# Kernel tuning notes

Measured on AMD Instinct MI355X. Metric: run time of the kernel, lower is better.

## Reference

```python
import jax, jax.numpy as jnp
import numpy as np

D_MODEL = 1040
N_HEADS = 16
FEAT = 32            # feature_dim
HEAD_DIM = 65        # d_model // num_heads; must equal 2*FEAT+1 for the z-division to broadcast
EPS = 1e-9


def setup_inputs() -> dict:
    key = jax.random.key(0)
    k1, k2, k3, k4, k5, k6 = jax.random.split(key, 6)
    B, S = 4, 4096
    scale = 1.0 / np.sqrt(D_MODEL)
    return {
        "hidden_states": jax.random.normal(k1, (B, S, D_MODEL), dtype=jnp.float32),
        "attention_mask": jax.random.randint(k2, (B, S), 0, 2, dtype=jnp.int32),
        "Wq": jax.random.normal(k3, (D_MODEL, N_HEADS * FEAT), dtype=jnp.float32) * scale,
        "Wk": jax.random.normal(k4, (D_MODEL, N_HEADS * FEAT), dtype=jnp.float32) * scale,
        "Wv": jax.random.normal(k5, (D_MODEL, N_HEADS * HEAD_DIM), dtype=jnp.float32) * scale,
        "Wo": jax.random.normal(k6, (N_HEADS * HEAD_DIM, D_MODEL), dtype=jnp.float32) * scale,
    }


def _phi(x):
    # polynomial feature map: [1, x, 0.5*x^2] -> last dim 2*FEAT+1
    return jnp.concatenate([jnp.ones_like(x[..., :1]), x, 0.5 * x * x], axis=-1)


def reference(hidden_states, attention_mask, Wq, Wk, Wv, Wo):
    B, S, _ = hidden_states.shape
    # projections -> [B, H, S, d]
    q = (hidden_states @ Wq).reshape(B, S, N_HEADS, FEAT).transpose(0, 2, 1, 3)
    k = (hidden_states @ Wk).reshape(B, S, N_HEADS, FEAT).transpose(0, 2, 1, 3)
    v = (hidden_states @ Wv).reshape(B, S, N_HEADS, HEAD_DIM).transpose(0, 2, 1, 3)
    q = _phi(q)  # [B, H, S, D] with D = 2*FEAT+1
    k = _phi(k)
    # linear attention: KV state then query it
    kv = jnp.einsum('bhnd,bhne->bhde', k, v)        # [B, H, D, HEAD_DIM]
    qkv = jnp.einsum('bhnd,bhde->bhne', q, kv)      # [B, H, S, HEAD_DIM]
    # z = einsum('bhnd,bhne->bhne', q, k.sum(n, keepdim)) with size-1 broadcast on n:
    # contracts d of q against k.sum's d-slot, i.e. (sum_d q) outer (sum_n k)
    z = jnp.sum(q, axis=-1, keepdims=True) * jnp.sum(k, axis=2, keepdims=True)  # [B,H,S,D]
    out = qkv / (z + EPS)                            # requires HEAD_DIM == D
    out = jnp.where(attention_mask[:, None, :, None] == 0, 0.0, out)
    out = out.transpose(0, 2, 1, 3).reshape(B, S, N_HEADS * HEAD_DIM)
    return out @ Wo
```

## Files before the change

kernel.cpp:

```cpp
#include <hip/hip_runtime.h>
#include <hip/hip_bf16.h>

typedef unsigned short ushort_t;
typedef unsigned int uint_t;

#define S_LEN 4096
#define BATCH 4
#define DMODEL 1040
#define KPAD 1056
#define KO 1152
#define NPADW 1152
#define M_TOK 16384
#define KVSPLIT 16

using f32x4 = __attribute__((ext_vector_type(4))) float;
using bf16x8 = __attribute__((ext_vector_type(8))) __bf16;
using f16x8 = __attribute__((ext_vector_type(8))) _Float16;

__device__ __forceinline__ void splitf16(float x, ushort_t& h, ushort_t& l) {
  _Float16 hf = (_Float16)x;
  float r = (x - (float)hf) * 4096.0f;
  _Float16 lf = (_Float16)r;
  h = __builtin_bit_cast(ushort_t, hf);
  l = __builtin_bit_cast(ushort_t, lf);
}

typedef const __attribute__((address_space(1))) unsigned int* gas_u32p;
typedef __attribute__((address_space(3))) unsigned int* las_u32p;
__device__ __forceinline__ void gload_lds16(const ushort_t* g, ushort_t* l) {
  __builtin_amdgcn_global_load_lds((gas_u32p)g, (las_u32p)l, 16, 0, 0);
}

__device__ __forceinline__ void tile_map(int lid, int NT, int PPX, int& m0, int& n0) {
  const int x = lid & 7, pos = lid >> 3;
  const int mi = pos / NT, ni = pos - mi * NT;
  m0 = (x * PPX + mi) * 128;
  n0 = ni * 128;
}

union pack8 { ushort_t u[8]; uint4 v; };

__global__ __launch_bounds__(256) void split_hs_kernel(const float* __restrict__ hs,
                                                       ushort_t* __restrict__ hh,
                                                       ushort_t* __restrict__ hl) {
  const int C8 = KPAD / 8;
  int idx = blockIdx.x * 256 + threadIdx.x;
  if (idx >= M_TOK * C8) return;
  int row = idx / C8, col = (idx % C8) * 8;
  pack8 ph, pl;
  if (col < DMODEL) {
    const float* p = &hs[(size_t)row * DMODEL + col];
#pragma unroll
    for (int j = 0; j < 8; ++j) splitf16(p[j], ph.u[j], pl.u[j]);
  } else {
#pragma unroll
    for (int j = 0; j < 8; ++j) { ph.u[j] = 0; pl.u[j] = 0; }
  }
  size_t o = (size_t)row * KPAD + col;
  *reinterpret_cast<uint4*>(&hh[o]) = ph.v;
  *reinterpret_cast<uint4*>(&hl[o]) = pl.v;
}

__global__ __launch_bounds__(256) void split_wqk_kernel(const float* __restrict__ Wq,
                                                        const float* __restrict__ Wk,
                                                        ushort_t* __restrict__ th,
                                                        ushort_t* __restrict__ tl) {
  const int C8 = KPAD / 8;
  int idx = blockIdx.x * 256 + threadIdx.x;
  if (idx >= 1024 * C8) return;
  int n = idx / C8, k = (idx % C8) * 8;
  pack8 ph, pl;
#pragma unroll
  for (int j = 0; j < 8; ++j) {
    int kk = k + j;
    float val = 0.f;
    if (kk < DMODEL) val = (n < 512) ? Wq[(size_t)kk * 512 + n] : Wk[(size_t)kk * 512 + (n - 512)];
    splitf16(val, ph.u[j], pl.u[j]);
  }
  size_t o = (size_t)n * KPAD + k;
  *reinterpret_cast<uint4*>(&th[o]) = ph.v;
  *reinterpret_cast<uint4*>(&tl[o]) = pl.v;
}

__global__ __launch_bounds__(256) void split_wv_kernel(const float* __restrict__ Wv,
                                                       ushort_t* __restrict__ th) {
  const int C8 = KPAD / 8;
  int idx = blockIdx.x * 256 + threadIdx.x;
  if (idx >= NPADW * C8) return;
  int n = idx / C8, k = (idx % C8) * 8;
  pack8 ph;
#pragma unroll
  for (int j = 0; j < 8; ++j) {
    int kk = k + j;
    float val = (n < DMODEL && kk < DMODEL) ? Wv[(size_t)kk * DMODEL + n] : 0.f;
    ph.u[j] = __builtin_bit_cast(ushort_t, (_Float16)val);
  }
  *reinterpret_cast<uint4*>(&th[(size_t)n * KPAD + k]) = ph.v;
}

__global__ __launch_bounds__(256) void split_wo_kernel(const float* __restrict__ Wo,
                                                       ushort_t* __restrict__ th) {
  const int C8O = KO / 8;
  int idx = blockIdx.x * 256 + threadIdx.x;
  if (idx >= NPADW * C8O) return;
  int n = idx / C8O, k = (idx % C8O) * 8;
  pack8 ph;
#pragma unroll
  for (int j = 0; j < 8; ++j) {
    int kk = k + j;
    int h = kk / 72, e = kk % 72;
    float val = (n < DMODEL && e < 65) ? Wo[(size_t)(h * 65 + e) * DMODEL + n] : 0.f;
    ph.u[j] = __builtin_bit_cast(ushort_t, __float2bfloat16(val));
  }
  *reinterpret_cast<uint4*>(&th[(size_t)n * KO + k]) = ph.v;
}

__global__ __launch_bounds__(512, 4) void gemm_qk(const ushort_t* __restrict__ Ahg,
                                                  const ushort_t* __restrict__ Alg,
                                                  const ushort_t* __restrict__ Bhg,
                                                  const ushort_t* __restrict__ Blg,
                                                  float* __restrict__ C, int kdim) {
  __shared__ ushort_t Ah[2][4096], Al[2][4096], Bh[2][4096], Bl[2][4096];
  const int t = threadIdx.x;
  const int w = t >> 6, l = t & 63;
  int m0, n0;
  tile_map(blockIdx.x, 8, 16, m0, n0);
  const int wm = w >> 2, wn = w & 3;
  const int row16 = l & 15, g = l >> 4;

  f32x4 acc[4][2], acc2[4][2];
#pragma unroll
  for (int m = 0; m < 4; ++m)
#pragma unroll
    for (int n = 0; n < 2; ++n) { acc[m][n] = (f32x4){0,0,0,0}; acc2[m][n] = (f32x4){0,0,0,0}; }

  const int chunk = t;
  const int r0 = chunk >> 2;
  const int ch0 = (chunk & 3) ^ ((r0 ^ (r0 >> 2)) & 3);

#define STAGE_QK(K0, BUF)                                                       \
  {                                                                             \
    const size_t ga = (size_t)(m0 + r0) * kdim + (K0) + ch0 * 8;                \
    const size_t gb = (size_t)(n0 + r0) * kdim + (K0) + ch0 * 8;                \
    gload_lds16(Ahg + ga, &Ah[BUF][chunk * 8]);                                 \
    gload_lds16(Alg + ga, &Al[BUF][chunk * 8]);                                 \
    gload_lds16(Bhg + gb, &Bh[BUF][chunk * 8]);                                 \
    gload_lds16(Blg + gb, &Bl[BUF][chunk * 8]);                                 \
  }

  STAGE_QK(0, 0);
  __syncthreads();
  for (int k0 = 0, it = 0; k0 < kdim; k0 += 32, ++it) {
    const int cur = it & 1;
    if (k0 + 32 < kdim) STAGE_QK(k0 + 32, cur ^ 1);
    f16x8 fah[4], fal[4], fbh[2], fbl[2];
#pragma unroll
    for (int f = 0; f < 4; ++f) {
      const int ra = wm * 64 + f * 16 + row16;
      const int ca = (g ^ ((ra ^ (ra >> 2)) & 3)) << 3;
      fah[f] = *(const f16x8*)&Ah[cur][ra * 32 + ca];
      fal[f] = *(const f16x8*)&Al[cur][ra * 32 + ca];
    }
#pragma unroll
    for (int f = 0; f < 2; ++f) {
      const int rb = wn * 32 + f * 16 + row16;
      const int cb = (g ^ ((rb ^ (rb >> 2)) & 3)) << 3;
      fbh[f] = *(const f16x8*)&Bh[cur][rb * 32 + cb];
      fbl[f] = *(const f16x8*)&Bl[cur][rb * 32 + cb];
    }
#pragma unroll
    for (int m = 0; m < 4; ++m)
#pragma unroll
      for (int n = 0; n < 2; ++n) {
        acc[m][n]  = __builtin_amdgcn_mfma_f32_16x16x32_f16(fah[m], fbh[n], acc[m][n], 0, 0, 0);
        acc2[m][n] = __builtin_amdgcn_mfma_f32_16x16x32_f16(fah[m], fbl[n], acc2[m][n], 0, 0, 0);
        acc2[m][n] = __builtin_amdgcn_mfma_f32_16x16x32_f16(fal[m], fbh[n], acc2[m][n], 0, 0, 0);
      }
    __syncthreads();
  }
#undef STAGE_QK

  const float S2 = 1.0f / 4096.0f;
#pragma unroll
  for (int m = 0; m < 4; ++m)
#pragma unroll
    for (int n = 0; n < 2; ++n) {
      const int col = n0 + wn * 32 + n * 16 + row16;
      const int rowb = m0 + wm * 64 + m * 16 + g * 4;
#pragma unroll
      for (int i = 0; i < 4; ++i)
        C[(size_t)(rowb + i) * 1024 + col] = acc[m][n][i] + acc2[m][n][i] * S2;
    }
}

__global__ __launch_bounds__(512, 4) void gemm_v(const ushort_t* __restrict__ Ahg,
                                                 const ushort_t* __restrict__ Bhg,
                                                 ushort_t* __restrict__ Cv, int kdim) {
  __shared__ ushort_t Ah[2][4096], Bh[2][4096];
  const int t = threadIdx.x;
  const int w = t >> 6, l = t & 63;
  int m0, n0;
  tile_map(blockIdx.x, 9, 16, m0, n0);
  const int wm = w >> 2, wn = w & 3;
  const int row16 = l & 15, g = l >> 4;

  f32x4 acc[4][2];
#pragma unroll
  for (int m = 0; m < 4; ++m)
#pragma unroll
    for (int n = 0; n < 2; ++n) acc[m][n] = (f32x4){0,0,0,0};

  const int chunk = t;
  const int r0 = chunk >> 2;
  const int ch0 = (chunk & 3) ^ ((r0 ^ (r0 >> 2)) & 3);

#define STAGE_V(K0, BUF)                                                        \
  {                                                                             \
    const size_t ga = (size_t)(m0 + r0) * kdim + (K0) + ch0 * 8;                \
    const size_t gb = (size_t)(n0 + r0) * kdim + (K0) + ch0 * 8;                \
    gload_lds16(Ahg + ga, &Ah[BUF][chunk * 8]);                                 \
    gload_lds16(Bhg + gb, &Bh[BUF][chunk * 8]);                                 \
  }

  STAGE_V(0, 0);
  __syncthreads();
  for (int k0 = 0, it = 0; k0 < kdim; k0 += 32, ++it) {
    const int cur = it & 1;
    if (k0 + 32 < kdim) STAGE_V(k0 + 32, cur ^ 1);
    f16x8 fah[4], fbh[2];
#pragma unroll
    for (int f = 0; f < 4; ++f) {
      const int ra = wm * 64 + f * 16 + row16;
      const int ca = (g ^ ((ra ^ (ra >> 2)) & 3)) << 3;
      fah[f] = *(const f16x8*)&Ah[cur][ra * 32 + ca];
    }
#pragma unroll
    for (int f = 0; f < 2; ++f) {
      const int rb = wn * 32 + f * 16 + row16;
      const int cb = (g ^ ((rb ^ (rb >> 2)) & 3)) << 3;
      fbh[f] = *(const f16x8*)&Bh[cur][rb * 32 + cb];
    }
#pragma unroll
    for (int m = 0; m < 4; ++m)
#pragma unroll
      for (int n = 0; n < 2; ++n)
        acc[m][n] = __builtin_amdgcn_mfma_f32_16x16x32_f16(fah[m], fbh[n], acc[m][n], 0, 0, 0);
    __syncthreads();
  }
#undef STAGE_V

#pragma unroll
  for (int m = 0; m < 4; ++m)
#pragma unroll
    for (int n = 0; n < 2; ++n) {
      const int col = n0 + wn * 32 + n * 16 + row16;
      const int rowb = m0 + wm * 64 + m * 16 + g * 4;
#pragma unroll
      for (int i = 0; i < 4; ++i)
        Cv[(size_t)(rowb + i) * 1152 + col] =
            __builtin_bit_cast(ushort_t, (_Float16)acc[m][n][i]);
    }
}

__global__ __launch_bounds__(512, 4) void gemm_o(const ushort_t* __restrict__ Ahg,
                                                 const ushort_t* __restrict__ Bhg,
                                                 float* __restrict__ C, int kdim) {
  __shared__ ushort_t Ah[2][4096], Bh[2][4096];
  const int t = threadIdx.x;
  const int w = t >> 6, l = t & 63;
  int m0, n0;
  tile_map(blockIdx.x, 9, 16, m0, n0);
  const int wm = w >> 2, wn = w & 3;
  const int row16 = l & 15, g = l >> 4;

  f32x4 acc[4][2];
#pragma unroll
  for (int m = 0; m < 4; ++m)
#pragma unroll
    for (int n = 0; n < 2; ++n) acc[m][n] = (f32x4){0,0,0,0};

  const int chunk = t;
  const int r0 = chunk >> 2;
  const int ch0 = (chunk & 3) ^ ((r0 ^ (r0 >> 2)) & 3);

#define STAGE_O(K0, BUF)                                                        \
  {                                                                             \
    const size_t ga = (size_t)(m0 + r0) * kdim + (K0) + ch0 * 8;                \
    const size_t gb = (size_t)(n0 + r0) * kdim + (K0) + ch0 * 8;                \
    gload_lds16(Ahg + ga, &Ah[BUF][chunk * 8]);                                 \
    gload_lds16(Bhg + gb, &Bh[BUF][chunk * 8]);                                 \
  }

  STAGE_O(0, 0);
  __syncthreads();
  for (int k0 = 0, it = 0; k0 < kdim; k0 += 32, ++it) {
    const int cur = it & 1;
    if (k0 + 32 < kdim) STAGE_O(k0 + 32, cur ^ 1);
    bf16x8 fah[4], fbh[2];
#pragma unroll
    for (int f = 0; f < 4; ++f) {
      const int ra = wm * 64 + f * 16 + row16;
      const int ca = (g ^ ((ra ^ (ra >> 2)) & 3)) << 3;
      fah[f] = *(const bf16x8*)&Ah[cur][ra * 32 + ca];
    }
#pragma unroll
    for (int f = 0; f < 2; ++f) {
      const int rb = wn * 32 + f * 16 + row16;
      const int cb = (g ^ ((rb ^ (rb >> 2)) & 3)) << 3;
      fbh[f] = *(const bf16x8*)&Bh[cur][rb * 32 + cb];
    }
#pragma unroll
    for (int m = 0; m < 4; ++m)
#pragma unroll
      for (int n = 0; n < 2; ++n)
        acc[m][n] = __builtin_amdgcn_mfma_f32_16x16x32_bf16(fah[m], fbh[n], acc[m][n], 0, 0, 0);
    __syncthreads();
  }
#undef STAGE_O

#pragma unroll
  for (int m = 0; m < 4; ++m)
#pragma unroll
    for (int n = 0; n < 2; ++n) {
      const int col = n0 + wn * 32 + n * 16 + row16;
      if (col < DMODEL) {
        const int rowb = m0 + wm * 64 + m * 16 + g * 4;
#pragma unroll
        for (int i = 0; i < 4; ++i) C[(size_t)(rowb + i) * DMODEL + col] = acc[m][n][i];
      }
    }
}

__global__ __launch_bounds__(256) void kv_kernel(const float* __restrict__ qk,
                                                 const ushort_t* __restrict__ vbuf,
                                                 float* __restrict__ kvpart,
                                                 float* __restrict__ kspart) {
  const int bh = blockIdx.x;
  const int split = blockIdx.y;
  const int b = bh >> 4, h = bh & 15;
  __shared__ float ks[64][68];
  __shared__ float vs[64][68];
  const int tid = threadIdx.x;
  const int d0 = (tid / 17) * 5;
  const int e0 = (tid % 17) * 4;
  const bool active = (tid < 221);
  float acc[5][4] = {};
  float kcol = 0.f;

  for (int chunk = 0; chunk < 4; ++chunk) {
    const int nb = split * 256 + chunk * 64;
    for (int idx = tid; idx < 64 * 65; idx += 256) {
      const int r = idx / 65, d = idx % 65;
      const size_t row = (size_t)(b * S_LEN + nb + r);
      float val;
      if (d == 0) val = 1.f;
      else if (d <= 32) val = qk[row * 1024 + 512 + h * 32 + (d - 1)];
      else {
        float x = qk[row * 1024 + 512 + h * 32 + (d - 33)];
        val = 0.5f * x * x;
      }
      ks[r][d] = val;
      vs[r][d] = (float)__builtin_bit_cast(_Float16, vbuf[row * 1152 + h * 65 + d]);
    }
    __syncthreads();
    if (active) {
      for (int r = 0; r < 64; ++r) {
        float a[5], v[4];
#pragma unroll
        for (int i = 0; i < 5; ++i) a[i] = ks[r][d0 + i];
#pragma unroll
        for (int j = 0; j < 4; ++j) v[j] = vs[r][e0 + j];
#pragma unroll
        for (int i = 0; i < 5; ++i)
#pragma unroll
          for (int j = 0; j < 4; ++j) acc[i][j] += a[i] * v[j];
      }
    }
    if (tid < 65) {
      float s = 0.f;
      for (int r = 0; r < 64; ++r) s += ks[r][tid];
      kcol += s;
    }
    __syncthreads();
  }

  if (active) {
    float* kvp = kvpart + ((size_t)split * 64 + bh) * 4225;
#pragma unroll
    for (int i = 0; i < 5; ++i)
#pragma unroll
      for (int j = 0; j < 4; ++j) {
        int e = e0 + j;
        if (e < 65) kvp[(d0 + i) * 65 + e] = acc[i][j];
      }
  }
  if (tid < 65) kspart[((size_t)split * 64 + bh) * 65 + tid] = kcol;
}

__global__ __launch_bounds__(256) void kv_reduce(const float* __restrict__ kvpart,
                                                 const float* __restrict__ kspart,
                                                 float* __restrict__ kv,
                                                 float* __restrict__ ksum) {
  const int NKV = 64 * 4225;
  const int NKS = 64 * 65;
  int i = blockIdx.x * 256 + threadIdx.x;
  if (i < NKV) {
    float s = 0.f;
#pragma unroll 8
    for (int p = 0; p < KVSPLIT; ++p) s += kvpart[(size_t)p * NKV + i];
    kv[i] = s;
  } else if (i < NKV + NKS) {
    int j = i - NKV;
    float s = 0.f;
#pragma unroll 8
    for (int p = 0; p < KVSPLIT; ++p) s += kspart[p * NKS + j];
    ksum[j] = s;
  }
}

__global__ __launch_bounds__(256) void qkv_kernel(const float* __restrict__ qk,
                                                  const float* __restrict__ kv,
                                                  const float* __restrict__ ksum,
                                                  const int* __restrict__ mask,
                                                  uint_t* __restrict__ ath32) {
  const int gx = blockIdx.x;
  const int bh = blockIdx.y;
  const int b = bh >> 4, h = bh & 15;
  __shared__ float kvs[65 * 68];
  __shared__ float phis[128][68];
  __shared__ float kss[65];
  __shared__ float qsums[128];
  const int tid = threadIdx.x;

  const float* kvp = kv + (size_t)bh * 4225;
  for (int i = tid; i < 4225; i += 256) kvs[(i / 65) * 68 + (i % 65)] = kvp[i];
  for (int idx = tid; idx < 128 * 32; idx += 256) {
    int tt = idx >> 5, f = idx & 31;
    size_t row = (size_t)(b * S_LEN + gx * 128 + tt);
    float val = qk[row * 1024 + h * 32 + f];
    phis[tt][1 + f] = val;
    phis[tt][33 + f] = 0.5f * val * val;
  }
  if (tid < 128) phis[tid][0] = 1.f;
  if (tid < 65) kss[tid] = ksum[bh * 65 + tid];
  __syncthreads();
  if (tid < 128) {
    float s = 0.f;
    for (int d = 0; d < 65; ++d) s += phis[tid][d];
    qsums[tid] = s;
  }
  __syncthreads();

  const int tt = tid >> 3, fg = tid & 7;
  float accs[4][8];
#pragma unroll
  for (int c = 0; c < 4; ++c)
#pragma unroll
    for (int j = 0; j < 8; ++j) accs[c][j] = 0.f;
  float a64[4] = {0.f, 0.f, 0.f, 0.f};

#pragma unroll 4
  for (int d = 0; d < 65; ++d) {
    const float* kr = &kvs[d * 68 + fg * 8];
    float4 va = *reinterpret_cast<const float4*>(kr);
    float4 vb = *reinterpret_cast<const float4*>(kr + 4);
    float kv64 = kvs[d * 68 + 64];
#pragma unroll
    for (int c = 0; c < 4; ++c) {
      float p = phis[c * 32 + tt][d];
      accs[c][0] += p * va.x; accs[c][1] += p * va.y;
      accs[c][2] += p * va.z; accs[c][3] += p * va.w;
      accs[c][4] += p * vb.x; accs[c][5] += p * vb.y;
      accs[c][6] += p * vb.z; accs[c][7] += p * vb.w;
      if (fg == 0) a64[c] += p * kv64;
    }
  }

#pragma unroll
  for (int c = 0; c < 4; ++c) {
    const int tok = c * 32 + tt;
    const int s_in_b = gx * 128 + tok;
    const size_t row = (size_t)(b * S_LEN + s_in_b);
    const int m = mask[b * S_LEN + s_in_b];
    const float qs = qsums[tok];
    const float fm = (m == 0) ? 0.f : 1.f;
    float o[8];
#pragma unroll
    for (int j = 0; j < 8; ++j) {
      float z = qs * kss[fg * 8 + j] + 1e-9f;
      o[j] = fm * accs[c][j] / z;
    }
    const size_t base = row * 576 + h * 36 + fg * 4;
    pack8 phh;
#pragma unroll
    for (int j = 0; j < 8; ++j)
      phh.u[j] = __builtin_bit_cast(ushort_t, __float2bfloat16(o[j]));
    *reinterpret_cast<uint4*>(&ath32[base]) = phh.v;
    if (fg == 0) {
      float z = qs * kss[64] + 1e-9f;
      float o64 = fm * a64[c] / z;
      uint4 tailh = {(uint_t)__builtin_bit_cast(ushort_t, __float2bfloat16(o64)), 0u, 0u, 0u};
      *reinterpret_cast<uint4*>(&ath32[row * 576 + h * 36 + 32]) = tailh;
    }
  }
}

extern "C" void kernel_launch(void* const* d_in, const int* in_sizes, int n_in,
                              void* d_out, int out_size, void* d_ws, size_t ws_size,
                              hipStream_t stream) {
  const float* hs = (const float*)d_in[0];
  const int* mask = (const int*)d_in[1];
  const float* Wq = (const float*)d_in[2];
  const float* Wk = (const float*)d_in[3];
  const float* Wv = (const float*)d_in[4];
  const float* Wo = (const float*)d_in[5];
  float* out = (float*)d_out;

  const size_t RA_BYTES = (size_t)M_TOK * KPAD * 2;
  const size_t RB_BYTES = (size_t)M_TOK * 1152 * 2;

  char* base = (char*)d_ws;
  ushort_t* hsh = (ushort_t*)base;
  float* kv = (float*)base;
  float* ksum = kv + 64 * 4225;
  float* kvpart = ksum + 64 * 65;
  float* kspart = kvpart + (size_t)KVSPLIT * 64 * 4225;
  char* rb = base + RA_BYTES;
  ushort_t* hsl = (ushort_t*)rb;
  ushort_t* vbuf = (ushort_t*)rb;
  uint_t* ath32 = (uint_t*)rb;
  char* rc = rb + RB_BYTES;
  float* qkbuf = (float*)rc;
  char* rw = rc + (size_t)M_TOK * 1024 * 4;
  ushort_t* Wqkh = (ushort_t*)rw;
  ushort_t* Wqkl = Wqkh + (size_t)1024 * KPAD;
  ushort_t* Wvh = Wqkl + (size_t)1024 * KPAD;
  ushort_t* Woh = Wvh + (size_t)NPADW * KPAD;

  dim3 blk(256);
  const int C8 = KPAD / 8;
  const int C8O = KO / 8;

  split_wqk_kernel<<<(1024 * C8 + 255) / 256, blk, 0, stream>>>(Wq, Wk, Wqkh, Wqkl);
  split_wv_kernel<<<(NPADW * C8 + 255) / 256, blk, 0, stream>>>(Wv, Wvh);
  split_wo_kernel<<<(NPADW * C8O + 255) / 256, blk, 0, stream>>>(Wo, Woh);

  split_hs_kernel<<<(M_TOK * C8 + 255) / 256, blk, 0, stream>>>(hs, hsh, hsl);

  gemm_qk<<<1024, dim3(512), 0, stream>>>(hsh, hsl, Wqkh, Wqkl, qkbuf, KPAD);
  gemm_v<<<1152, dim3(512), 0, stream>>>(hsh, Wvh, vbuf, KPAD);

  kv_kernel<<<dim3(64, KVSPLIT), blk, 0, stream>>>(qkbuf, vbuf, kvpart, kspart);
  kv_reduce<<<(64 * 4225 + 64 * 65 + 255) / 256, blk, 0, stream>>>(kvpart, kspart, kv, ksum);

  qkv_kernel<<<dim3(32, 64), blk, 0, stream>>>(qkbuf, kv, ksum, mask, ath32);

  gemm_o<<<1152, dim3(512), 0, stream>>>((ushort_t*)ath32, Woh, out, KO);
}
```

Before: 429.6 us.

## Pad V heads to 72 columns and vectorize kv_kernel tile loads

Reorders the packed Wv weight so each head's 65 value columns start on a 72-aligned stride, which makes the V projection output head-aligned. kv_kernel then loads K features and V values with 16-byte vector loads per thread, replacing the scalar per-element gather with its div/mod and branches. The gain is expected in the KV-state reduction's global-load phase. Other consumers of vbuf (qkv/output stages not shown) must also agree on the new 72-stride layout, which is a consistency risk.

```diff
diff --git a/kernel.cpp b/kernel.cpp
--- a/kernel.cpp
+++ b/kernel.cpp
@@ -88,11 +88,12 @@
   int idx = blockIdx.x * 256 + threadIdx.x;
   if (idx >= NPADW * C8) return;
   int n = idx / C8, k = (idx % C8) * 8;
+  int hh_ = n / 72, e = n % 72;
   pack8 ph;
 #pragma unroll
   for (int j = 0; j < 8; ++j) {
     int kk = k + j;
-    float val = (n < DMODEL && kk < DMODEL) ? Wv[(size_t)kk * DMODEL + n] : 0.f;
+    float val = (e < 65 && kk < DMODEL) ? Wv[(size_t)kk * DMODEL + (hh_ * 65 + e)] : 0.f;
     ph.u[j] = __builtin_bit_cast(ushort_t, (_Float16)val);
   }
   *reinterpret_cast<uint4*>(&th[(size_t)n * KPAD + k]) = ph.v;
@@ -341,6 +342,8 @@
   __shared__ float ks[64][68];
   __shared__ float vs[64][68];
   const int tid = threadIdx.x;
+  const int fr = tid >> 2;
+  const int fp = tid & 3;
   const int d0 = (tid / 17) * 5;
   const int e0 = (tid % 17) * 4;
   const bool active = (tid < 221);
@@ -349,18 +352,29 @@
 
   for (int chunk = 0; chunk < 4; ++chunk) {
     const int nb = split * 256 + chunk * 64;
-    for (int idx = tid; idx < 64 * 65; idx += 256) {
-      const int r = idx / 65, d = idx % 65;
-      const size_t row = (size_t)(b * S_LEN + nb + r);
-      float val;
-      if (d == 0) val = 1.f;
-      else if (d <= 32) val = qk[row * 1024 + 512 + h * 32 + (d - 1)];
-      else {
-        float x = qk[row * 1024 + 512 + h * 32 + (d - 33)];
-        val = 0.5f * x * x;
+    {
+      const size_t row = (size_t)(b * S_LEN + nb + fr);
+      const float* kx = &qk[row * 1024 + 512 + h * 32 + fp * 8];
+      float4 x0 = *reinterpret_cast<const float4*>(kx);
+      float4 x1 = *reinterpret_cast<const float4*>(kx + 4);
+      float xs[8] = {x0.x, x0.y, x0.z, x0.w, x1.x, x1.y, x1.z, x1.w};
+#pragma unroll
+      for (int j = 0; j < 8; ++j) {
+        ks[fr][1 + fp * 8 + j] = xs[j];
+        ks[fr][33 + fp * 8 + j] = 0.5f * xs[j] * xs[j];
       }
-      ks[r][d] = val;
-      vs[r][d] = (float)__builtin_bit_cast(_Float16, vbuf[row * 1152 + h * 65 + d]);
+      if (fp == 0) ks[fr][0] = 1.f;
+      const ushort_t* vp = &vbuf[row * 1152 + h * 72 + fp * 16];
+      uint4 v0 = *reinterpret_cast<const uint4*>(vp);
+      uint4 v1 = *reinterpret_cast<const uint4*>(vp + 8);
+      const ushort_t* vu0 = reinterpret_cast<const ushort_t*>(&v0);
+      const ushort_t* vu1 = reinterpret_cast<const ushort_t*>(&v1);
+#pragma unroll
+      for (int j = 0; j < 8; ++j) {
+        vs[fr][fp * 16 + j] = (float)__builtin_bit_cast(_Float16, vu0[j]);
+        vs[fr][fp * 16 + 8 + j] = (float)__builtin_bit_cast(_Float16, vu1[j]);
+      }
+      if (fp == 3) vs[fr][64] = (float)__builtin_bit_cast(_Float16, vbuf[row * 1152 + h * 72 + 64]);
     }
     __syncthreads();
     if (active) {
```

Result: faster. 407.3 us (-5.2%).
